# Performance work log

Hardware: AMD Instinct MI355X
Metric: run time of the kernel (lower is better)

## Reference

```python
import jax, jax.numpy as jnp
import numpy as np

B, N, K = 4, 4096, 32
NIN, RANK, NOUT, HID = 64, 16, 128, 64
EPS = 1e-7


def _ln(x, g, b, eps=1e-5):
    mu = jnp.mean(x, axis=-1, keepdims=True)
    var = jnp.mean((x - mu) ** 2, axis=-1, keepdims=True)
    return (x - mu) * jax.lax.rsqrt(var + eps) * g + b


def _zm(a):
    c, s = jnp.cos(a), jnp.sin(a)
    z, o = jnp.zeros_like(a), jnp.ones_like(a)
    return jnp.stack([c, -s, z, s, c, z, z, z, o], -1).reshape(*a.shape, 3, 3)


def _ym(a):
    c, s = jnp.cos(a), jnp.sin(a)
    z, o = jnp.zeros_like(a), jnp.ones_like(a)
    return jnp.stack([c, z, s, z, o, z, -s, z, c], -1).reshape(*a.shape, 3, 3)


def _rifeat(points_r, points_s):
    # points_r: (B,N,K,3); points_s: (B,N,1,3)
    r_mean = jnp.mean(points_r, axis=-2, keepdims=True)
    l1 = r_mean - points_r
    l2 = points_r - points_s
    l3 = points_s - r_mean  # (B,N,1,3)
    l1n = jnp.linalg.norm(l1, axis=-1, keepdims=True)
    l2n = jnp.linalg.norm(l2, axis=-1, keepdims=True)
    l3n = jnp.linalg.norm(l3, axis=-1, keepdims=True)  # (B,N,1,1)
    theta1 = jnp.sum(l1 * l2, -1, keepdims=True) / (l1n * l2n + EPS)
    theta2 = jnp.sum(l2 * l3, -1, keepdims=True) / (l2n * l3n + EPS)
    theta3 = jnp.sum(l3 * l1, -1, keepdims=True) / (l3n * l1n + EPS)
    # spherical angles of eval point; torch code swaps channels [0,2] then negates
    az = jnp.arctan2(points_s[..., 1], points_s[..., 0])          # (B,N,1)
    pol = jnp.arccos(jnp.clip(points_s[..., 2] / jnp.linalg.norm(points_s, axis=-1), -1.0, 1.0))
    sx = jnp.stack([-points_s[..., 2], -pol, -az], -1)            # (B,N,1,3)
    m = (_zm(sx[..., 0]) @ _ym(sx[..., 1]) @ _zm(sx[..., 2]))[:, :, 0]  # (B,N,3,3)
    h = jnp.linalg.norm(points_r, axis=-1, keepdims=True)         # (B,N,K,1)
    r_s2 = points_r / h
    res = jnp.einsum('bnxy,bnky->bnkx', m, r_s2)
    txj = jnp.arccos(jnp.clip(res[..., 2:3], -1.0, 1.0)) / np.pi
    l3n_b = jnp.broadcast_to(l3n, l1n.shape)
    return jnp.concatenate([txj, h, l1n, l2n, l3n_b, theta1, theta2, theta3], -1)  # (B,N,K,8)


def setup_inputs() -> dict:
    key = jax.random.key(0)
    ks = jax.random.split(key, 12)
    rn = lambda k, shape, s=1.0: jax.random.normal(k, shape, jnp.float32) * s
    return {
        'feat_points': rn(ks[0], (B, N, K, 3)),
        'feat': rn(ks[1], (B, N, K, NIN)),
        'eval_points': rn(ks[2], (B, N, 3)),
        # kernel MLP: Linear(8->HID) + LN + ReLU + Linear(HID->RANK)
        'w1': rn(ks[3], (8, HID), 1.0 / np.sqrt(8.0)),
        'b1': rn(ks[4], (HID,), 0.02),
        'g1': jnp.ones((HID,), jnp.float32),
        'be1': jnp.zeros((HID,), jnp.float32),
        'w2': rn(ks[5], (HID, RANK), 1.0 / np.sqrt(HID)),
        'b2': rn(ks[6], (RANK,), 0.02),
        # outnet: Linear(RANK*NIN -> NOUT)
        'wo': rn(ks[7], (RANK * NIN, NOUT), 1.0 / np.sqrt(RANK * NIN)),
        'bwo': rn(ks[8], (NOUT,), 0.02),
        # final LayerNorm
        'gln': jnp.ones((NOUT,), jnp.float32),
        'bln': jnp.zeros((NOUT,), jnp.float32),
    }


def reference(feat_points, feat, eval_points, w1, b1, g1, be1, w2, b2, wo, bwo, gln, bln):
    points_s = eval_points[:, :, None, :]                 # (B,N,1,3)
    ri = _rifeat(feat_points, points_s)                   # (B,N,K,8)
    hdn = jax.nn.relu(_ln(ri @ w1 + b1, g1, be1))         # (B,N,K,HID)
    kern = hdn @ w2 + b2                                  # (B,N,K,RANK)
    contracted = jnp.einsum('bnkr,bnki->bnri', kern, feat)
    contracted = contracted.reshape(feat.shape[0], feat.shape[1], -1)  # (B,N,RANK*NIN)
    out = contracted @ wo + bwo                           # (B,N,NOUT)
    return _ln(out, gln, bln)
```

## Files before the change

### kernel.cpp

```cpp
#include <hip/hip_runtime.h>
#include <hip/hip_bf16.h>

#define KP    32
#define NIN_  64
#define RNK   16
#define NOUT_ 128
#define HID_  64
#define CDIM  1024
#define EPS_  1e-7f
#define LNEPS 1e-5f
#define NTOT  16384

using short8 = __attribute__((ext_vector_type(8))) short;
using f32x4  = __attribute__((ext_vector_type(4))) float;

#define GLD16(gsrc, ldst) __builtin_amdgcn_global_load_lds( \
    (const __attribute__((address_space(1))) void*)(gsrc),  \
    (__attribute__((address_space(3))) void*)(ldst), 16, 0, 0)

__device__ __forceinline__ unsigned short f2bf(float x) {
  unsigned u = __float_as_uint(x);
  return (unsigned short)((u + 0x7fffu + ((u >> 16) & 1u)) >> 16);
}
__device__ __forceinline__ float rsum8(float v) {
  v += __shfl_xor(v, 1); v += __shfl_xor(v, 2); v += __shfl_xor(v, 4);
  return v;
}

__global__ __launch_bounds__(256) void k0_woT(const float* __restrict__ wo,
                                              unsigned short* __restrict__ woT) {
  __shared__ unsigned short S[64][129];
  const int t = threadIdx.x;
  const int k0 = blockIdx.x * 64;
  #pragma unroll
  for (int i = 0; i < 32; ++i) {
    const int idx = i * 256 + t;
    const int k = idx >> 7, n = idx & 127;
    S[k][n] = f2bf(wo[(long)(k0 + k) * NOUT_ + n]);
  }
  __syncthreads();
  #pragma unroll
  for (int i = 0; i < 32; ++i) {
    const int idx = i * 256 + t;
    const int n = idx >> 6, k = idx & 63;
    woT[(long)n * CDIM + k0 + k] = S[k][n];
  }
}

__global__ __launch_bounds__(256) void k1_contract(
    const float* __restrict__ fp,
    const float* __restrict__ feat,
    const float* __restrict__ ep,
    const float* __restrict__ w1,
    const float* __restrict__ b1, const float* __restrict__ g1,
    const float* __restrict__ be1,
    const float* __restrict__ w2,
    const float* __restrict__ b2,
    unsigned short* __restrict__ A)
{
  __shared__ __align__(16) float featS[KP * NIN_];
  __shared__ __align__(16) float w1T[64][8];
  __shared__ __align__(16) float w2T[16][68];
  __shared__ __align__(16) float riS[KP][8];
  __shared__ __align__(16) float hdnS[KP][68];
  __shared__ __align__(16) float kern2[KP * RNK];

  const int t = threadIdx.x;
  const long bn = blockIdx.x;

  const float* fsrc = feat + bn * (KP * NIN_);
  GLD16(fsrc + t * 4, featS + t * 4);
  GLD16(fsrc + (t + 256) * 4, featS + (t + 256) * 4);

  if (t < 64) {
    #pragma unroll
    for (int x = 0; x < 8; ++x) w1T[t][x] = w1[x * HID_ + t];
  }
  #pragma unroll
  for (int i = 0; i < 4; ++i) {
    const int idx = t + 256 * i;
    const int r = idx >> 6, hh = idx & 63;
    w2T[r][hh] = w2[hh * RNK + r];
  }

  if (t < KP) {
    const float* prp = fp + (bn * KP + t) * 3;
    float prx = prp[0], pry = prp[1], prz = prp[2];
    const float* psp = ep + bn * 3;
    float psx = psp[0], psy = psp[1], psz = psp[2];

    float sx = prx, sy = pry, sz = prz;
    #pragma unroll
    for (int m = 16; m >= 1; m >>= 1) {
      sx += __shfl_xor(sx, m); sy += __shfl_xor(sy, m); sz += __shfl_xor(sz, m);
    }
    const float inv = 1.f / 32.f;
    float mx = sx * inv, my = sy * inv, mz = sz * inv;

    float l1x = mx - prx, l1y = my - pry, l1z = mz - prz;
    float l2x = prx - psx, l2y = pry - psy, l2z = prz - psz;
    float l3x = psx - mx, l3y = psy - my, l3z = psz - mz;
    float l1n = sqrtf(l1x * l1x + l1y * l1y + l1z * l1z);
    float l2n = sqrtf(l2x * l2x + l2y * l2y + l2z * l2z);
    float l3n = sqrtf(l3x * l3x + l3y * l3y + l3z * l3z);
    float th1 = (l1x * l2x + l1y * l2y + l1z * l2z) / (l1n * l2n + EPS_);
    float th2 = (l2x * l3x + l2y * l3y + l2z * l3z) / (l2n * l3n + EPS_);
    float th3 = (l3x * l1x + l3y * l1y + l3z * l1z) / (l3n * l1n + EPS_);
    float h   = sqrtf(prx * prx + pry * pry + prz * prz);
    float psn = sqrtf(psx * psx + psy * psy + psz * psz);
    float c = (psx * prx + psy * pry + psz * prz) / (psn * h);
    c = fminf(1.f, fmaxf(-1.f, c));
    float txj = acosf(c) * 0.31830988618379067f;

    riS[t][0] = txj; riS[t][1] = h;   riS[t][2] = l1n; riS[t][3] = l2n;
    riS[t][4] = l3n; riS[t][5] = th1; riS[t][6] = th2; riS[t][7] = th3;
  }
  __syncthreads();

  {
    const int k = t >> 3, s = t & 7;
    const float4 rv0 = *reinterpret_cast<const float4*>(&riS[k][0]);
    const float4 rv1 = *reinterpret_cast<const float4*>(&riS[k][4]);
    float vals[8];
    #pragma unroll
    for (int j = 0; j < 8; ++j) {
      const int hh = s + 8 * j;
      const float4 wv0 = *reinterpret_cast<const float4*>(&w1T[hh][0]);
      const float4 wv1 = *reinterpret_cast<const float4*>(&w1T[hh][4]);
      vals[j] = b1[hh]
        + rv0.x * wv0.x + rv0.y * wv0.y + rv0.z * wv0.z + rv0.w * wv0.w
        + rv1.x * wv1.x + rv1.y * wv1.y + rv1.z * wv1.z + rv1.w * wv1.w;
    }
    float psum = 0.f;
    #pragma unroll
    for (int j = 0; j < 8; ++j) psum += vals[j];
    const float mu = rsum8(psum) * (1.f / 64.f);
    float vsum = 0.f;
    #pragma unroll
    for (int j = 0; j < 8; ++j) { float d = vals[j] - mu; vsum += d * d; }
    const float rstd = rsqrtf(rsum8(vsum) * (1.f / 64.f) + LNEPS);
    #pragma unroll
    for (int j = 0; j < 8; ++j) {
      const int hh = s + 8 * j;
      hdnS[k][hh] = fmaxf((vals[j] - mu) * rstd * g1[hh] + be1[hh], 0.f);
    }
  }
  __syncthreads();

  #pragma unroll
  for (int it = 0; it < 2; ++it) {
    const int idx = t + 256 * it;
    const int k = idx >> 4, r = idx & 15;
    float a = b2[r];
    #pragma unroll
    for (int h0 = 0; h0 < HID_; h0 += 4) {
      const float4 hv = *reinterpret_cast<const float4*>(&hdnS[k][h0]);
      const float4 wv = *reinterpret_cast<const float4*>(&w2T[r][h0]);
      a += hv.x * wv.x + hv.y * wv.y + hv.z * wv.z + hv.w * wv.w;
    }
    kern2[k * RNK + r] = a;
  }
  __syncthreads();

  if (t < 128) {
    const int rp = t >> 4, iq = t & 15;
    float a00 = 0.f, a01 = 0.f, a02 = 0.f, a03 = 0.f;
    float a10 = 0.f, a11 = 0.f, a12 = 0.f, a13 = 0.f;
    #pragma unroll 8
    for (int k = 0; k < KP; ++k) {
      const float4 fv = *reinterpret_cast<const float4*>(&featS[k * NIN_ + iq * 4]);
      const float2 kv = *reinterpret_cast<const float2*>(&kern2[k * RNK + rp * 2]);
      a00 += kv.x * fv.x; a01 += kv.x * fv.y; a02 += kv.x * fv.z; a03 += kv.x * fv.w;
      a10 += kv.y * fv.x; a11 += kv.y * fv.y; a12 += kv.y * fv.z; a13 += kv.y * fv.w;
    }
    unsigned short* Ab = A + bn * CDIM;
    ushort4 o0 = make_ushort4(f2bf(a00), f2bf(a01), f2bf(a02), f2bf(a03));
    ushort4 o1 = make_ushort4(f2bf(a10), f2bf(a11), f2bf(a12), f2bf(a13));
    *reinterpret_cast<ushort4*>(&Ab[(rp * 2 + 0) * NIN_ + iq * 4]) = o0;
    *reinterpret_cast<ushort4*>(&Ab[(rp * 2 + 1) * NIN_ + iq * 4]) = o1;
  }
}

__global__ __launch_bounds__(256) void k2_gemm_ln(
    const unsigned short* __restrict__ A,
    const unsigned short* __restrict__ woT,
    const float* __restrict__ bwo, const float* __restrict__ gln,
    const float* __restrict__ bln, float* __restrict__ out)
{
  __shared__ __align__(16) unsigned short As[64 * 64];
  __shared__ __align__(16) unsigned short Bs[128 * 64];
  __shared__ __align__(16) float Cs[64 * 132];

  const int t = threadIdx.x;
  const int w = t >> 6, l = t & 63;
  const int mw = w & 1, nw = w >> 1;
  const long row0 = (long)blockIdx.x * 64;

  f32x4 acc[2][4];
  #pragma unroll
  for (int mt = 0; mt < 2; ++mt)
    #pragma unroll
    for (int nt = 0; nt < 4; ++nt) acc[mt][nt] = (f32x4){0.f, 0.f, 0.f, 0.f};

  for (int k0 = 0; k0 < CDIM; k0 += 64) {
    #pragma unroll
    for (int i = 0; i < 2; ++i) {
      const int idx = t + 256 * i;
      const int row = idx >> 3, c = idx & 7;
      const int cs = c ^ (row & 7);
      GLD16(A + (row0 + row) * CDIM + k0 + cs * 8, As + idx * 8);
    }
    #pragma unroll
    for (int i = 0; i < 4; ++i) {
      const int idx = t + 256 * i;
      const int row = idx >> 3, c = idx & 7;
      const int cs = c ^ (row & 7);
      GLD16(woT + (long)row * CDIM + k0 + cs * 8, Bs + idx * 8);
    }
    __syncthreads();

    const int kg = l >> 4, m = l & 15;
    #pragma unroll
    for (int ks = 0; ks < 2; ++ks) {
      const int kc = ks * 4 + kg;
      short8 af[2], bfr[4];
      #pragma unroll
      for (int mt = 0; mt < 2; ++mt) {
        const int row = mw * 32 + mt * 16 + m;
        af[mt] = *reinterpret_cast<const short8*>(&As[row * 64 + ((kc ^ (row & 7)) << 3)]);
      }
      #pragma unroll
      for (int nt = 0; nt < 4; ++nt) {
        const int row = nw * 64 + nt * 16 + m;
        bfr[nt] = *reinterpret_cast<const short8*>(&Bs[row * 64 + ((kc ^ (row & 7)) << 3)]);
      }
      #pragma unroll
      for (int mt = 0; mt < 2; ++mt)
        #pragma unroll
        for (int nt = 0; nt < 4; ++nt)
          acc[mt][nt] = __builtin_amdgcn_mfma_f32_16x16x32_bf16(
              af[mt], bfr[nt], acc[mt][nt], 0, 0, 0);
    }
    __syncthreads();
  }

  #pragma unroll
  for (int mt = 0; mt < 2; ++mt)
    #pragma unroll
    for (int nt = 0; nt < 4; ++nt)
      #pragma unroll
      for (int r = 0; r < 4; ++r) {
        const int row = mw * 32 + mt * 16 + (l >> 4) * 4 + r;
        const int col = nw * 64 + nt * 16 + (l & 15);
        Cs[row * 132 + col] = acc[mt][nt][r];
      }
  __syncthreads();

  {
    const int row = t >> 2, q = t & 3;
    float4 v[8];
    #pragma unroll
    for (int i = 0; i < 8; ++i) {
      float4 cv = *reinterpret_cast<const float4*>(&Cs[row * 132 + q * 32 + i * 4]);
      const float4 bv = *reinterpret_cast<const float4*>(&bwo[q * 32 + i * 4]);
      v[i] = make_float4(cv.x + bv.x, cv.y + bv.y, cv.z + bv.z, cv.w + bv.w);
    }
    float s = 0.f;
    #pragma unroll
    for (int i = 0; i < 8; ++i) s += v[i].x + v[i].y + v[i].z + v[i].w;
    s += __shfl_xor(s, 1); s += __shfl_xor(s, 2);
    const float mu = s * (1.f / 128.f);
    float d2 = 0.f;
    #pragma unroll
    for (int i = 0; i < 8; ++i) {
      float dx = v[i].x - mu, dy = v[i].y - mu, dz = v[i].z - mu, dw = v[i].w - mu;
      d2 += dx * dx + dy * dy + dz * dz + dw * dw;
    }
    d2 += __shfl_xor(d2, 1); d2 += __shfl_xor(d2, 2);
    const float rstd = rsqrtf(d2 * (1.f / 128.f) + LNEPS);
    float* op = out + (row0 + row) * NOUT_ + q * 32;
    #pragma unroll
    for (int i = 0; i < 8; ++i) {
      const float4 gv = *reinterpret_cast<const float4*>(&gln[q * 32 + i * 4]);
      const float4 bv = *reinterpret_cast<const float4*>(&bln[q * 32 + i * 4]);
      float4 o;
      o.x = (v[i].x - mu) * rstd * gv.x + bv.x;
      o.y = (v[i].y - mu) * rstd * gv.y + bv.y;
      o.z = (v[i].z - mu) * rstd * gv.z + bv.z;
      o.w = (v[i].w - mu) * rstd * gv.w + bv.w;
      *reinterpret_cast<float4*>(op + i * 4) = o;
    }
  }
}

extern "C" void kernel_launch(void* const* d_in, const int* in_sizes, int n_in,
                              void* d_out, int out_size, void* d_ws, size_t ws_size,
                              hipStream_t stream) {
  const float* fp   = (const float*)d_in[0];
  const float* feat = (const float*)d_in[1];
  const float* ep   = (const float*)d_in[2];
  const float* w1   = (const float*)d_in[3];
  const float* b1   = (const float*)d_in[4];
  const float* g1   = (const float*)d_in[5];
  const float* be1  = (const float*)d_in[6];
  const float* w2   = (const float*)d_in[7];
  const float* b2   = (const float*)d_in[8];
  const float* wo   = (const float*)d_in[9];
  const float* bwo  = (const float*)d_in[10];
  const float* gln  = (const float*)d_in[11];
  const float* bln  = (const float*)d_in[12];
  float* out = (float*)d_out;

  unsigned short* A   = (unsigned short*)d_ws;
  unsigned short* woT = (unsigned short*)((char*)d_ws + (48u << 20));

  k0_woT<<<16, 256, 0, stream>>>(wo, woT);
  k1_contract<<<NTOT, 256, 0, stream>>>(fp, feat, ep, w1, b1, g1, be1, w2, b2, A);
  k2_gemm_ln<<<NTOT / 64, 256, 0, stream>>>(A, woT, bwo, gln, bln, out);
}
```

Baseline: 323.5 us.

## Restructure contraction kernel to wave-per-point loop and double-buffer GEMM loads

The contraction kernel now gives each wavefront four points in turn, with 16 points per block and 1024 blocks. Every lane computes the geometric features and MLP for half of one neighbour in registers, which removes most block-wide barriers and the idle threads of the old one-point-per-block design. Each wave copies its own feat tile to shared memory asynchronously and waits on vmcnt only before the contraction step. The output GEMM kernel now double-buffers its A and B tiles so global loads overlap the MFMAs, and reuses the staging shared memory for the epilogue. The trade-off is higher register use (32 hidden values plus 16 kernel accumulators per lane) and more shared memory per block, which may lower occupancy.

```diff
diff --git a/kernel.cpp b/kernel.cpp
--- a/kernel.cpp
+++ b/kernel.cpp
@@ -21,10 +21,6 @@
 __device__ __forceinline__ unsigned short f2bf(float x) {
   unsigned u = __float_as_uint(x);
   return (unsigned short)((u + 0x7fffu + ((u >> 16) & 1u)) >> 16);
-}
-__device__ __forceinline__ float rsum8(float v) {
-  v += __shfl_xor(v, 1); v += __shfl_xor(v, 2); v += __shfl_xor(v, 4);
-  return v;
 }
 
 __global__ __launch_bounds__(256) void k0_woT(const float* __restrict__ wo,
@@ -58,126 +54,135 @@
     const float* __restrict__ b2,
     unsigned short* __restrict__ A)
 {
-  __shared__ __align__(16) float featS[KP * NIN_];
-  __shared__ __align__(16) float w1T[64][8];
-  __shared__ __align__(16) float w2T[16][68];
-  __shared__ __align__(16) float riS[KP][8];
-  __shared__ __align__(16) float hdnS[KP][68];
-  __shared__ __align__(16) float kern2[KP * RNK];
+  __shared__ float w1T[64][8];
+  __shared__ float w2S[64][16];
+  __shared__ float b1S[64], g1S[64], beS[64], b2S[16];
+  __shared__ __align__(16) float featW[4][KP * NIN_];
+  __shared__ float kernS[4][KP][17];
 
   const int t = threadIdx.x;
-  const long bn = blockIdx.x;
-
-  const float* fsrc = feat + bn * (KP * NIN_);
-  GLD16(fsrc + t * 4, featS + t * 4);
-  GLD16(fsrc + (t + 256) * 4, featS + (t + 256) * 4);
+  const int wv = t >> 6, lane = t & 63;
+  const int hh = lane & 1, kk = lane >> 1;
 
   if (t < 64) {
     #pragma unroll
     for (int x = 0; x < 8; ++x) w1T[t][x] = w1[x * HID_ + t];
-  }
-  #pragma unroll
-  for (int i = 0; i < 4; ++i) {
-    const int idx = t + 256 * i;
-    const int r = idx >> 6, hh = idx & 63;
-    w2T[r][hh] = w2[hh * RNK + r];
-  }
-
-  if (t < KP) {
-    const float* prp = fp + (bn * KP + t) * 3;
+    b1S[t] = b1[t]; g1S[t] = g1[t]; beS[t] = be1[t];
+  }
+  reinterpret_cast<float4*>(&w2S[0][0])[t] = reinterpret_cast<const float4*>(w2)[t];
+  if (t < 16) b2S[t] = b2[t];
+  __syncthreads();
+
+  #pragma unroll 1
+  for (int pi = 0; pi < 4; ++pi) {
+    const long pt = (long)blockIdx.x * 16 + wv * 4 + pi;
+
+    __builtin_amdgcn_sched_barrier(0);
+    {
+      const float* fsrc = feat + pt * (KP * NIN_);
+      float* fdst = &featW[wv][0];
+      #pragma unroll
+      for (int j = 0; j < 8; ++j)
+        GLD16(fsrc + j * 256 + lane * 4, fdst + j * 256 + lane * 4);
+    }
+
+    const float* prp = fp + (pt * KP + kk) * 3;
     float prx = prp[0], pry = prp[1], prz = prp[2];
-    const float* psp = ep + bn * 3;
+    const float* psp = ep + pt * 3;
     float psx = psp[0], psy = psp[1], psz = psp[2];
 
     float sx = prx, sy = pry, sz = prz;
     #pragma unroll
-    for (int m = 16; m >= 1; m >>= 1) {
+    for (int m = 2; m <= 32; m <<= 1) {
       sx += __shfl_xor(sx, m); sy += __shfl_xor(sy, m); sz += __shfl_xor(sz, m);
     }
     const float inv = 1.f / 32.f;
-    float mx = sx * inv, my = sy * inv, mz = sz * inv;
-
-    float l1x = mx - prx, l1y = my - pry, l1z = mz - prz;
-    float l2x = prx - psx, l2y = pry - psy, l2z = prz - psz;
-    float l3x = psx - mx, l3y = psy - my, l3z = psz - mz;
-    float l1n = sqrtf(l1x * l1x + l1y * l1y + l1z * l1z);
-    float l2n = sqrtf(l2x * l2x + l2y * l2y + l2z * l2z);
-    float l3n = sqrtf(l3x * l3x + l3y * l3y + l3z * l3z);
-    float th1 = (l1x * l2x + l1y * l2y + l1z * l2z) / (l1n * l2n + EPS_);
-    float th2 = (l2x * l3x + l2y * l3y + l2z * l3z) / (l2n * l3n + EPS_);
-    float th3 = (l3x * l1x + l3y * l1y + l3z * l1z) / (l3n * l1n + EPS_);
-    float h   = sqrtf(prx * prx + pry * pry + prz * prz);
-    float psn = sqrtf(psx * psx + psy * psy + psz * psz);
-    float c = (psx * prx + psy * pry + psz * prz) / (psn * h);
+    const float mx = sx * inv, my = sy * inv, mz = sz * inv;
+
+    const float l1x = mx - prx, l1y = my - pry, l1z = mz - prz;
+    const float l2x = prx - psx, l2y = pry - psy, l2z = prz - psz;
+    const float l3x = psx - mx, l3y = psy - my, l3z = psz - mz;
+    const float l1n = sqrtf(l1x * l1x + l1y * l1y + l1z * l1z);
+    const float l2n = sqrtf(l2x * l2x + l2y * l2y + l2z * l2z);
+    const float l3n = sqrtf(l3x * l3x + l3y * l3y + l3z * l3z);
+    const float th1 = (l1x * l2x + l1y * l2y + l1z * l2z) / (l1n * l2n + EPS_);
+    const float th2 = (l2x * l3x + l2y * l3y + l2z * l3z) / (l2n * l3n + EPS_);
+    const float th3 = (l3x * l1x + l3y * l1y + l3z * l1z) / (l3n * l1n + EPS_);
+    const float hn  = sqrtf(prx * prx + pry * pry + prz * prz);
+    const float psn = sqrtf(psx * psx + psy * psy + psz * psz);
+    float c = (psx * prx + psy * pry + psz * prz) / (psn * hn);
     c = fminf(1.f, fmaxf(-1.f, c));
-    float txj = acosf(c) * 0.31830988618379067f;
-
-    riS[t][0] = txj; riS[t][1] = h;   riS[t][2] = l1n; riS[t][3] = l2n;
-    riS[t][4] = l3n; riS[t][5] = th1; riS[t][6] = th2; riS[t][7] = th3;
-  }
-  __syncthreads();
-
-  {
-    const int k = t >> 3, s = t & 7;
-    const float4 rv0 = *reinterpret_cast<const float4*>(&riS[k][0]);
-    const float4 rv1 = *reinterpret_cast<const float4*>(&riS[k][4]);
-    float vals[8];
-    #pragma unroll
-    for (int j = 0; j < 8; ++j) {
-      const int hh = s + 8 * j;
-      const float4 wv0 = *reinterpret_cast<const float4*>(&w1T[hh][0]);
-      const float4 wv1 = *reinterpret_cast<const float4*>(&w1T[hh][4]);
-      vals[j] = b1[hh]
-        + rv0.x * wv0.x + rv0.y * wv0.y + rv0.z * wv0.z + rv0.w * wv0.w
-        + rv1.x * wv1.x + rv1.y * wv1.y + rv1.z * wv1.z + rv1.w * wv1.w;
-    }
-    float psum = 0.f;
-    #pragma unroll
-    for (int j = 0; j < 8; ++j) psum += vals[j];
-    const float mu = rsum8(psum) * (1.f / 64.f);
-    float vsum = 0.f;
-    #pragma unroll
-    for (int j = 0; j < 8; ++j) { float d = vals[j] - mu; vsum += d * d; }
-    const float rstd = rsqrtf(rsum8(vsum) * (1.f / 64.f) + LNEPS);
-    #pragma unroll
-    for (int j = 0; j < 8; ++j) {
-      const int hh = s + 8 * j;
-      hdnS[k][hh] = fmaxf((vals[j] - mu) * rstd * g1[hh] + be1[hh], 0.f);
-    }
-  }
-  __syncthreads();
-
-  #pragma unroll
-  for (int it = 0; it < 2; ++it) {
-    const int idx = t + 256 * it;
-    const int k = idx >> 4, r = idx & 15;
-    float a = b2[r];
-    #pragma unroll
-    for (int h0 = 0; h0 < HID_; h0 += 4) {
-      const float4 hv = *reinterpret_cast<const float4*>(&hdnS[k][h0]);
-      const float4 wv = *reinterpret_cast<const float4*>(&w2T[r][h0]);
-      a += hv.x * wv.x + hv.y * wv.y + hv.z * wv.z + hv.w * wv.w;
-    }
-    kern2[k * RNK + r] = a;
-  }
-  __syncthreads();
-
-  if (t < 128) {
-    const int rp = t >> 4, iq = t & 15;
-    float a00 = 0.f, a01 = 0.f, a02 = 0.f, a03 = 0.f;
-    float a10 = 0.f, a11 = 0.f, a12 = 0.f, a13 = 0.f;
+    const float ri0 = acosf(c) * 0.31830988618379067f;
+    const float ri1 = hn,  ri2 = l1n, ri3 = l2n;
+    const float ri4 = l3n, ri5 = th1, ri6 = th2, ri7 = th3;
+
+    float vals[32];
+    #pragma unroll
+    for (int j = 0; j < 32; ++j) {
+      const int h = hh * 32 + j;
+      const float4 wa = *reinterpret_cast<const float4*>(&w1T[h][0]);
+      const float4 wb = *reinterpret_cast<const float4*>(&w1T[h][4]);
+      vals[j] = b1S[h]
+        + ri0 * wa.x + ri1 * wa.y + ri2 * wa.z + ri3 * wa.w
+        + ri4 * wb.x + ri5 * wb.y + ri6 * wb.z + ri7 * wb.w;
+    }
+    float s = 0.f;
+    #pragma unroll
+    for (int j = 0; j < 32; ++j) s += vals[j];
+    s += __shfl_xor(s, 1);
+    const float mu = s * (1.f / 64.f);
+    float v2 = 0.f;
+    #pragma unroll
+    for (int j = 0; j < 32; ++j) { const float d = vals[j] - mu; v2 += d * d; }
+    v2 += __shfl_xor(v2, 1);
+    const float rstd = rsqrtf(v2 * (1.f / 64.f) + LNEPS);
+    #pragma unroll
+    for (int j = 0; j < 32; ++j) {
+      const int h = hh * 32 + j;
+      vals[j] = fmaxf((vals[j] - mu) * rstd * g1S[h] + beS[h], 0.f);
+    }
+
+    float kern[16];
+    #pragma unroll
+    for (int r = 0; r < 16; ++r) kern[r] = 0.f;
+    #pragma unroll
+    for (int j = 0; j < 32; ++j) {
+      const int h = hh * 32 + j;
+      const float hv = vals[j];
+      #pragma unroll
+      for (int rc = 0; rc < 4; ++rc) {
+        const float4 wr = *reinterpret_cast<const float4*>(&w2S[h][rc * 4]);
+        kern[rc * 4 + 0] += hv * wr.x;
+        kern[rc * 4 + 1] += hv * wr.y;
+        kern[rc * 4 + 2] += hv * wr.z;
+        kern[rc * 4 + 3] += hv * wr.w;
+      }
+    }
+    #pragma unroll
+    for (int r = 0; r < 16; ++r) kern[r] += __shfl_xor(kern[r], 1);
+    #pragma unroll
+    for (int q = 0; q < 8; ++q)
+      kernS[wv][kk][hh * 8 + q] = kern[hh * 8 + q] + b2S[hh * 8 + q];
+
+    asm volatile("s_waitcnt vmcnt(0)" ::: "memory");
+    __builtin_amdgcn_sched_barrier(0);
+    const int rr = lane & 15, riq = lane >> 4;
+    f32x4 a0 = {0.f,0.f,0.f,0.f}, a1 = a0, a2 = a0, a3 = a0;
     #pragma unroll 8
-    for (int k = 0; k < KP; ++k) {
-      const float4 fv = *reinterpret_cast<const float4*>(&featS[k * NIN_ + iq * 4]);
-      const float2 kv = *reinterpret_cast<const float2*>(&kern2[k * RNK + rp * 2]);
-      a00 += kv.x * fv.x; a01 += kv.x * fv.y; a02 += kv.x * fv.z; a03 += kv.x * fv.w;
-      a10 += kv.y * fv.x; a11 += kv.y * fv.y; a12 += kv.y * fv.z; a13 += kv.y * fv.w;
-    }
-    unsigned short* Ab = A + bn * CDIM;
-    ushort4 o0 = make_ushort4(f2bf(a00), f2bf(a01), f2bf(a02), f2bf(a03));
-    ushort4 o1 = make_ushort4(f2bf(a10), f2bf(a11), f2bf(a12), f2bf(a13));
-    *reinterpret_cast<ushort4*>(&Ab[(rp * 2 + 0) * NIN_ + iq * 4]) = o0;
-    *reinterpret_cast<ushort4*>(&Ab[(rp * 2 + 1) * NIN_ + iq * 4]) = o1;
+    for (int kq = 0; kq < 32; ++kq) {
+      const float kv = kernS[wv][kq][rr];
+      const float* fb = &featW[wv][kq * 64 + riq * 4];
+      const f32x4 f0 = *reinterpret_cast<const f32x4*>(fb);
+      const f32x4 f1 = *reinterpret_cast<const f32x4*>(fb + 16);
+      const f32x4 f2 = *reinterpret_cast<const f32x4*>(fb + 32);
+      const f32x4 f3 = *reinterpret_cast<const f32x4*>(fb + 48);
+      a0 += kv * f0; a1 += kv * f1; a2 += kv * f2; a3 += kv * f3;
+    }
+    unsigned short* Ap = A + pt * CDIM + rr * 64 + riq * 4;
+    *reinterpret_cast<ushort4*>(Ap +  0) = make_ushort4(f2bf(a0[0]), f2bf(a0[1]), f2bf(a0[2]), f2bf(a0[3]));
+    *reinterpret_cast<ushort4*>(Ap + 16) = make_ushort4(f2bf(a1[0]), f2bf(a1[1]), f2bf(a1[2]), f2bf(a1[3]));
+    *reinterpret_cast<ushort4*>(Ap + 32) = make_ushort4(f2bf(a2[0]), f2bf(a2[1]), f2bf(a2[2]), f2bf(a2[3]));
+    *reinterpret_cast<ushort4*>(Ap + 48) = make_ushort4(f2bf(a3[0]), f2bf(a3[1]), f2bf(a3[2]), f2bf(a3[3]));
   }
 }
 
@@ -187,9 +192,10 @@
     const float* __restrict__ bwo, const float* __restrict__ gln,
     const float* __restrict__ bln, float* __restrict__ out)
 {
-  __shared__ __align__(16) unsigned short As[64 * 64];
-  __shared__ __align__(16) unsigned short Bs[128 * 64];
-  __shared__ __align__(16) float Cs[64 * 132];
+  __shared__ __align__(16) char smem[49152];
+  unsigned short* AsB = reinterpret_cast<unsigned short*>(smem);
+  unsigned short* BsB = reinterpret_cast<unsigned short*>(smem + 16384);
+  float* Cs = reinterpret_cast<float*>(smem);
 
   const int t = threadIdx.x;
   const int w = t >> 6, l = t & 63;
@@ -202,23 +208,35 @@
     #pragma unroll
     for (int nt = 0; nt < 4; ++nt) acc[mt][nt] = (f32x4){0.f, 0.f, 0.f, 0.f};
 
-  for (int k0 = 0; k0 < CDIM; k0 += 64) {
+  auto stage = [&](int buf, int k0) {
+    unsigned short* Ad = AsB + buf * 4096;
+    unsigned short* Bd = BsB + buf * 8192;
     #pragma unroll
     for (int i = 0; i < 2; ++i) {
       const int idx = t + 256 * i;
       const int row = idx >> 3, c = idx & 7;
       const int cs = c ^ (row & 7);
-      GLD16(A + (row0 + row) * CDIM + k0 + cs * 8, As + idx * 8);
+      GLD16(A + (row0 + row) * CDIM + k0 + cs * 8, Ad + idx * 8);
     }
     #pragma unroll
     for (int i = 0; i < 4; ++i) {
       const int idx = t + 256 * i;
       const int row = idx >> 3, c = idx & 7;
       const int cs = c ^ (row & 7);
-      GLD16(woT + (long)row * CDIM + k0 + cs * 8, Bs + idx * 8);
-    }
-    __syncthreads();
-
+      GLD16(woT + (long)row * CDIM + k0 + cs * 8, Bd + idx * 8);
+    }
+  };
+
+  stage(0, 0);
+  asm volatile("s_waitcnt vmcnt(0)" ::: "memory");
+  __builtin_amdgcn_s_barrier();
+
+  for (int c = 0; c < 16; ++c) {
+    const int cur = c & 1;
+    if (c < 15) stage(cur ^ 1, (c + 1) * 64);
+
+    const unsigned short* Ab = AsB + cur * 4096;
+    const unsigned short* Bb = BsB + cur * 8192;
     const int kg = l >> 4, m = l & 15;
     #pragma unroll
     for (int ks = 0; ks < 2; ++ks) {
@@ -227,12 +245,12 @@
       #pragma unroll
       for (int mt = 0; mt < 2; ++mt) {
         const int row = mw * 32 + mt * 16 + m;
-        af[mt] = *reinterpret_cast<const short8*>(&As[row * 64 + ((kc ^ (row & 7)) << 3)]);
+        af[mt] = *reinterpret_cast<const short8*>(&Ab[row * 64 + ((kc ^ (row & 7)) << 3)]);
       }
       #pragma unroll
       for (int nt = 0; nt < 4; ++nt) {
         const int row = nw * 64 + nt * 16 + m;
-        bfr[nt] = *reinterpret_cast<const short8*>(&Bs[row * 64 + ((kc ^ (row & 7)) << 3)]);
+        bfr[nt] = *reinterpret_cast<const short8*>(&Bb[row * 64 + ((kc ^ (row & 7)) << 3)]);
       }
       #pragma unroll
       for (int mt = 0; mt < 2; ++mt)
@@ -241,7 +259,8 @@
           acc[mt][nt] = __builtin_amdgcn_mfma_f32_16x16x32_bf16(
               af[mt], bfr[nt], acc[mt][nt], 0, 0, 0);
     }
-    __syncthreads();
+    asm volatile("s_waitcnt vmcnt(0)" ::: "memory");
+    __builtin_amdgcn_s_barrier();
   }
 
   #pragma unroll
@@ -261,7 +280,7 @@
     float4 v[8];
     #pragma unroll
     for (int i = 0; i < 8; ++i) {
-      float4 cv = *reinterpret_cast<const float4*>(&Cs[row * 132 + q * 32 + i * 4]);
+      const float4 cv = *reinterpret_cast<const float4*>(&Cs[row * 132 + q * 32 + i * 4]);
       const float4 bv = *reinterpret_cast<const float4*>(&bwo[q * 32 + i * 4]);
       v[i] = make_float4(cv.x + bv.x, cv.y + bv.y, cv.z + bv.z, cv.w + bv.w);
     }
@@ -273,7 +292,7 @@
     float d2 = 0.f;
     #pragma unroll
     for (int i = 0; i < 8; ++i) {
-      float dx = v[i].x - mu, dy = v[i].y - mu, dz = v[i].z - mu, dw = v[i].w - mu;
+      const float dx = v[i].x - mu, dy = v[i].y - mu, dz = v[i].z - mu, dw = v[i].w - mu;
       d2 += dx * dx + dy * dy + dz * dz + dw * dw;
     }
     d2 += __shfl_xor(d2, 1); d2 += __shfl_xor(d2, 2);
@@ -315,6 +334,6 @@
   unsigned short* woT = (unsigned short*)((char*)d_ws + (48u << 20));
 
   k0_woT<<<16, 256, 0, stream>>>(wo, woT);
-  k1_contract<<<NTOT, 256, 0, stream>>>(fp, feat, ep, w1, b1, g1, be1, w2, b2, A);
+  k1_contract<<<1024, 256, 0, stream>>>(fp, feat, ep, w1, b1, g1, be1, w2, b2, A);
   k2_gemm_ln<<<NTOT / 64, 256, 0, stream>>>(A, woT, bwo, gln, bln, out);
 }
```

New measurement: 295.5 us. 1.09x faster.
